# Kernel tuning notes

Hardware: AMD Instinct MI355X
Metric: run time of the kernel (lower is better)

## Reference

```python
import jax, jax.numpy as jnp
import numpy as np

NUM_CLASSES = 19
IGNORE = 255
KLD_MARGIN = 3.0
DEC = 0.01
BOT_EPS, TOP_EPS = 1e-4, 1.0
# eight-corner neighbor offsets (size=1), order matches AAF layers.eightcorner_activation
EDGE_OFFS = ((-1, -1), (-1, 0), (-1, 1), (0, -1), (0, 1), (1, -1), (1, 0), (1, 1))


def _shift(x, dy, dx, pad_val):
    # Shift along H,W (axes 1,2): out[:, y, x] = x[:, y+dy, x+dx], padded with pad_val.
    pads = [(0, 0), (1, 1), (1, 1)] + [(0, 0)] * (x.ndim - 3)
    xp = jnp.pad(x, pads, constant_values=pad_val)
    h, w = x.shape[1], x.shape[2]
    return xp[:, 1 + dy:1 + dy + h, 1 + dx:1 + dx + w]


def _resize_bilinear_ac(x, oh, ow):
    # torch F.interpolate(mode='bilinear', align_corners=True) on NCHW.
    n, c, h, w = x.shape
    ys = jnp.linspace(0.0, h - 1.0, oh)
    xs = jnp.linspace(0.0, w - 1.0, ow)
    y0 = jnp.floor(ys).astype(jnp.int32); y1 = jnp.minimum(y0 + 1, h - 1)
    x0 = jnp.floor(xs).astype(jnp.int32); x1 = jnp.minimum(x0 + 1, w - 1)
    wy = (ys - y0).astype(x.dtype)[None, None, :, None]
    wx = (xs - x0).astype(x.dtype)[None, None, None, :]
    rows = x[:, :, y0, :] * (1.0 - wy) + x[:, :, y1, :] * wy  # (N,C,oh,W)
    return rows[:, :, :, x0] * (1.0 - wx) + rows[:, :, :, x1] * wx  # (N,C,oh,ow)


def setup_inputs() -> dict:
    key = jax.random.key(0)
    k1, k2 = jax.random.split(key)
    preds = jax.random.normal(k1, (2, NUM_CLASSES, 64, 64), dtype=jnp.float32)
    targets = jax.random.randint(k2, (2, 512, 512), 0, NUM_CLASSES, dtype=jnp.int32)
    w_edge = jnp.zeros((1, 1, 1, NUM_CLASSES, 1, 3), dtype=jnp.float32)
    w_not_edge = jnp.zeros((1, 1, 1, NUM_CLASSES, 1, 3), dtype=jnp.float32)
    return {"preds": preds, "targets": targets, "w_edge": w_edge, "w_not_edge": w_not_edge}


def reference(preds, targets, w_edge, w_not_edge):
    h, w = targets.shape[1], targets.shape[2]
    pred = _resize_bilinear_ac(preds, h, w)          # (N,C,H,W)
    prob = jax.nn.softmax(pred, axis=1)
    prob = jnp.transpose(prob, (0, 2, 3, 1))          # (N,H,W,C) NHWC layout used by AAF layers

    labels = targets                                  # (N,H,W)
    ign = labels == IGNORE
    one_label = jnp.where(ign, 0, labels)
    ohl = jax.nn.one_hot(one_label, NUM_CLASSES, dtype=jnp.float32)  # (N,H,W,C)
    ohl = jnp.where(ign[..., None], float(IGNORE), ohl)

    # edge/non-edge class weights: softmax over last dim, take index 0 -> (1,1,1,C,1)
    w_e = jax.nn.softmax(w_edge, axis=-1)[..., 0]
    w_ne = jax.nn.softmax(w_not_edge, axis=-1)[..., 0]

    # ignores_from_label: bidirectional ignore mask, neighbor order is reversed offsets
    ignore_c = labels > NUM_CLASSES - 1               # (N,H,W)
    ignore8 = jnp.stack([_shift(ignore_c, -dy, -dx, True) | ignore_c for dy, dx in EDGE_OFFS], axis=-1)
    not_ignore = ~ignore8[:, :, :, None, :]           # (N,H,W,1,8)

    # edges_from_label: neighbor label (padded with ignore_class) differs from center
    edge8 = jnp.stack([_shift(ohl, dy, dx, float(IGNORE)) != ohl for dy, dx in EDGE_OFFS], axis=-1)  # (N,H,W,C,8)
    edge = edge8 & not_ignore
    not_edge = (~edge) & not_ignore

    # eightcorner_activation on probabilities (zero padded)
    probs_paired = jnp.stack([_shift(prob, dy, dx, 0.0) for dy, dx in EDGE_OFFS], axis=-1)  # (N,H,W,C,8)
    p = prob[..., None]                               # (N,H,W,C,1)
    pc = jnp.clip(p, BOT_EPS, TOP_EPS)
    npc = jnp.clip(1.0 - p, BOT_EPS, TOP_EPS)
    ppc = jnp.clip(probs_paired, BOT_EPS, TOP_EPS)
    nppc = jnp.clip(1.0 - probs_paired, BOT_EPS, TOP_EPS)

    # binary KL divergence per class/neighbor
    kldiv = ppc * jnp.log(ppc / pc) + nppc * jnp.log(nppc / npc)  # (N,H,W,C,8)

    # per-pixel class weights: sum_c w[c]*one_hot[c] -> (N,H,W,1,1)
    we_map = jnp.sum(w_e * ohl[..., None], axis=3, keepdims=True)
    wne_map = jnp.sum(w_ne * ohl[..., None], axis=3, keepdims=True)

    edge_loss = jnp.maximum(0.0, KLD_MARGIN - kldiv) * we_map
    not_edge_loss = kldiv * wne_map

    # torch.mean over gathered nonzero indices == masked sum / count
    e_cnt = jnp.maximum(jnp.sum(edge), 1).astype(jnp.float32)
    ne_cnt = jnp.maximum(jnp.sum(not_edge), 1).astype(jnp.float32)
    e_mean = jnp.sum(jnp.where(edge, edge_loss, 0.0)) / e_cnt
    ne_mean = jnp.sum(jnp.where(not_edge, not_edge_loss, 0.0)) / ne_cnt

    return e_mean * 1.0 * DEC + ne_mean * 1.0 * DEC
```

## Files before the change

kernel.cpp:

```cpp
#include <hip/hip_runtime.h>
#include <stdint.h>


#define NC 19
#define HH 512
#define WW 512
#define NB 2
#define TS 16
#define HS 18
#define HP (HS * HS)
#define ATRS 28
#define PS 25
#define NBLK2 1024
#define LOGEPS -9.210340371976182f

typedef _Float16 f16x2 __attribute__((ext_vector_type(2)));

#if __has_builtin(__builtin_amdgcn_fdot2)
#define FDOT2(a, b, c) __builtin_amdgcn_fdot2((a), (b), (c), false)
#else
#define FDOT2(a, b, c) fmaf((float)(a)[1], (float)(b)[1], fmaf((float)(a)[0], (float)(b)[0], (c)))
#endif

struct Part { float es, ns; unsigned int cnt, pad; };

union U32F2 { uint32_t u; f16x2 h; };
__device__ __forceinline__ uint32_t bc_u32(f16x2 v) { U32F2 x; x.h = v; return x.u; }
__device__ __forceinline__ f16x2 bc_h2(uint32_t v) { U32F2 x; x.u = v; return x.h; }
__device__ __forceinline__ float extf(f16x2 v, int h) { return h ? (float)v[1] : (float)v[0]; }

template <bool KEEP>
__device__ __forceinline__ int pix_compute(const float* __restrict__ patch,
                                           const int* __restrict__ tg,
                                           int y, int x, int y0b, int x0b,
                                           uint32_t* __restrict__ ATrow,
                                           f16x2* Dh, f16x2* Lh) {
    const bool oob = ((unsigned)y >= (unsigned)HH) | ((unsigned)x >= (unsigned)WW);
    if (oob) {
        const _Float16 aP = (_Float16)1e-4f, dP = (_Float16)LOGEPS;
        const _Float16 tP = (_Float16)((float)aP * (float)dP);
        const uint32_t aPP = bc_u32((f16x2){aP, aP});
        const uint32_t tPP = bc_u32((f16x2){tP, tP});
        const uint32_t aPL = bc_u32((f16x2){aP, (_Float16)0.0f});
        const uint32_t tPL = bc_u32((f16x2){tP, (_Float16)0.0f});
#pragma unroll
        for (int i = 0; i < 5; ++i) {
            uint4 wv;
            wv.x = aPP; wv.y = tPP;
            wv.z = (i < 4) ? aPP : aPL;
            wv.w = (i < 4) ? tPP : tPL;
            *reinterpret_cast<uint4*>(ATrow + 4 * i) = wv;
            if (KEEP) {
                Dh[2 * i] = (f16x2){dP, dP};
                Dh[2 * i + 1] = (i < 4) ? (f16x2){dP, dP} : (f16x2){dP, (_Float16)0.0f};
                Lh[2 * i] = (f16x2){(_Float16)0.0f, (_Float16)0.0f};
                Lh[2 * i + 1] = (f16x2){(_Float16)0.0f, (_Float16)0.0f};
            }
        }
        return 255;
    }

    const int lab = tg[(y << 9) + x];
    const float fy = (float)(y * 63) / 511.0f;
    const float fx = (float)(x * 63) / 511.0f;
    const int y0 = (int)fy, x0 = (int)fx;
    const float wy = fy - (float)y0, wx = fx - (float)x0;
    const int y1 = min(y0 + 1, 63), x1 = min(x0 + 1, 63);
    const float omwy = 1.0f - wy, omwx = 1.0f - wx;
    const int o00 = (y0 - y0b) * 5 + (x0 - x0b);
    const int o01 = (y0 - y0b) * 5 + (x1 - x0b);
    const int o10 = (y1 - y0b) * 5 + (x0 - x0b);
    const int o11 = (y1 - y0b) * 5 + (x1 - x0b);

    float v[NC], w[NC];
    float m = -1e30f;
#pragma unroll
    for (int c = 0; c < NC; ++c) {
        const float* pc_ = &patch[c * PS];
        const float a = pc_[o00] * omwy + pc_[o10] * wy;
        const float b = pc_[o01] * omwy + pc_[o11] * wy;
        const float vv = a * omwx + b * wx;
        v[c] = vv;
        m = fmaxf(m, vv);
    }
    float s = 0.0f;
#pragma unroll
    for (int c = 0; c < NC; ++c) { w[c] = __expf(v[c] - m); s += w[c]; }
    const float inv = 1.0f / s;
    const float lns = __logf(s) + m;

#pragma unroll
    for (int i = 0; i < 5; ++i) {
        _Float16 av[4], tv[4], dv[4], lv[4];
#pragma unroll
        for (int q = 0; q < 4; ++q) {
            const int c = 4 * i + q;
            _Float16 a16 = (_Float16)0.0f, d16 = (_Float16)0.0f,
                     l16 = (_Float16)0.0f, t16 = (_Float16)0.0f;
            if (c < NC) {
                const float p = w[c] * inv;
                const float la = fmaxf(v[c] - lns, LOGEPS);
                const float aa = fmaxf(p, 1e-4f);
                const float lb = __logf(fmaxf(1.0f - p, 1e-4f));
                a16 = (_Float16)aa;
                d16 = (_Float16)(la - lb);
                l16 = (_Float16)lb;
                t16 = (_Float16)fmaf((float)a16, (float)d16, (float)l16);
            }
            av[q] = a16; tv[q] = t16; dv[q] = d16; lv[q] = l16;
        }
        uint4 wv;
        wv.x = bc_u32((f16x2){av[0], av[1]});
        wv.y = bc_u32((f16x2){tv[0], tv[1]});
        wv.z = bc_u32((f16x2){av[2], av[3]});
        wv.w = bc_u32((f16x2){tv[2], tv[3]});
        *reinterpret_cast<uint4*>(ATrow + 4 * i) = wv;
        if (KEEP) {
            Dh[2 * i] = (f16x2){dv[0], dv[1]};
            Dh[2 * i + 1] = (f16x2){dv[2], dv[3]};
            Lh[2 * i] = (f16x2){lv[0], lv[1]};
            Lh[2 * i + 1] = (f16x2){lv[2], lv[3]};
        }
    }
    return lab;
}

__global__ __launch_bounds__(256, 4) void k_fused(const float* __restrict__ preds,
                                                  const int* __restrict__ targets,
                                                  const float* __restrict__ w_edge,
                                                  const float* __restrict__ w_not_edge,
                                                  Part* __restrict__ pb) {
    __shared__ __align__(16) uint32_t AT[HP * ATRS];
    __shared__ int   TG[HP];
    __shared__ float swe[NC], swn[NC];
    __shared__ float patch[NC * PS];
    __shared__ float r_es[4], r_ns[4];
    __shared__ unsigned int r_cnt[4];

    const int tid = threadIdx.x;
    const int bx = blockIdx.x, n = blockIdx.z;

    if (tid < NC) {
        {
            float a = w_edge[tid * 3 + 0], b = w_edge[tid * 3 + 1], c = w_edge[tid * 3 + 2];
            float m = fmaxf(a, fmaxf(b, c));
            float ea = __expf(a - m), eb = __expf(b - m), ec = __expf(c - m);
            swe[tid] = ea / (ea + eb + ec);
        }
        {
            float a = w_not_edge[tid * 3 + 0], b = w_not_edge[tid * 3 + 1], c = w_not_edge[tid * 3 + 2];
            float m = fmaxf(a, fmaxf(b, c));
            float ea = __expf(a - m), eb = __expf(b - m), ec = __expf(c - m);
            swn[tid] = ea / (ea + eb + ec);
        }
    }

    const int* tg = targets + (n << 18);
    const float* pbase = preds + (size_t)n * NC * 4096;

    const int ty = tid >> 4, tx = tid & 15;
    const int hi = (ty + 1) * HS + (tx + 1);
    const int DOFF[8] = {-HS - 1, -HS, -HS + 1, -1, 1, HS - 1, HS, HS + 1};
    const f16x2 one2 = {(_Float16)1.0f, (_Float16)1.0f};
    const f16x2 k32 = {(_Float16)3.0f, (_Float16)3.0f};
    const f16x2 z2 = {(_Float16)0.0f, (_Float16)0.0f};

    float e_s = 0.0f, ne_s = 0.0f;
    unsigned int cnt = 0;

    for (int half = 0; half < 2; ++half) {
        const int by = blockIdx.y + 16 * half;
        if (half) __syncthreads();

        const int yT = max(by * TS - 1, 0), xL = max(bx * TS - 1, 0);
        const int y0b = (yT * 63) / 511, x0b = (xL * 63) / 511;
        for (int t = tid; t < NC * PS; t += 256) {
            const int c = t / PS, r = t - c * PS;
            const int ry = r / 5, rx = r - ry * 5;
            const int sy = min(y0b + ry, 63), sx = min(x0b + rx, 63);
            patch[t] = pbase[c * 4096 + (sy << 6) + sx];
        }
        __syncthreads();

        if (tid < 68) {
            int i;
            if (tid < 18)      i = tid;
            else if (tid < 36) i = 306 + (tid - 18);
            else if (tid < 52) i = (tid - 35) * HS;
            else               i = (tid - 51) * HS + 17;
            const int hy = i / HS, hx = i - hy * HS;
            TG[i] = pix_compute<false>(patch, tg, by * TS + hy - 1, bx * TS + hx - 1,
                                       y0b, x0b, &AT[i * ATRS], nullptr, nullptr);
        }

        f16x2 Dh[10], Lh[10];
        const int lab = pix_compute<true>(patch, tg, by * TS + ty, bx * TS + tx,
                                          y0b, x0b, &AT[hi * ATRS], Dh, Lh);
        TG[hi] = lab;
        __syncthreads();

        const bool interior_blk = (bx > 0) & (bx < 31) & (by > 0) & (by < 31);
        const int plab = lab >> 1, hlab = lab & 1;
        float es_h = 0.0f, ns_h = 0.0f;
        unsigned int cnt_h = 0;

        if (interior_blk) {
#pragma unroll
            for (int k = 0; k < 8; ++k) {
                const int np = hi + DOFF[k];
                const int nlab = TG[np];
                const int pn = nlab >> 1, hn = nlab & 1;
                const uint32_t* wbp = &AT[np * ATRS];
                float dot0 = 0.0f, dot1 = 0.0f;
                f16x2 klLw = z2, klNw = z2;
#pragma unroll
                for (int i = 0; i < 5; ++i) {
                    const uint4 rd = *reinterpret_cast<const uint4*>(wbp + 4 * i);
                    const int j0 = 2 * i, j1 = 2 * i + 1;
                    const f16x2 kl20 = bc_h2(rd.y) - (bc_h2(rd.x) * Dh[j0] + Lh[j0]);
                    const f16x2 kl21 = bc_h2(rd.w) - (bc_h2(rd.z) * Dh[j1] + Lh[j1]);
                    dot0 = FDOT2(kl20, one2, dot0);
                    dot1 = FDOT2(kl21, one2, dot1);
                    klLw = (j0 == plab) ? kl20 : klLw;
                    klLw = (j1 == plab) ? kl21 : klLw;
                    klNw = (j0 == pn) ? kl20 : klNw;
                    klNw = (j1 == pn) ? kl21 : klNw;
                }
                const float dot = dot0 + dot1;
                const float klL = extf(klLw, hlab);
                const float klN = extf(klNw, hn);
                const bool df = (lab != nlab);
                const float w = df ? 1.0f : 0.0f;
                es_h = fmaf(w, fmaxf(3.0f - klL, 0.0f) + fmaxf(3.0f - klN, 0.0f), es_h);
                ns_h += dot - w * (klL + klN);
                cnt_h += df ? ((2u << 16) | (NC - 2)) : NC;
            }
            e_s = fmaf(es_h, swe[lab], e_s);
            ne_s = fmaf(ns_h, swn[lab], ne_s);
            cnt += cnt_h;
        } else if (lab <= NC - 1) {
#pragma unroll
            for (int k = 0; k < 8; ++k) {
                const int off = DOFF[k];
                const int rlab = TG[hi - off];
                const int np = hi + off;
                const int nlab = TG[np];
                const int pn = nlab >> 1, hn = nlab & 1;
                const uint32_t* wbp = &AT[np * ATRS];
                float dot0 = 0.0f, dot1 = 0.0f, ekall = 0.0f;
                f16x2 klLw = z2, klNw = z2;
#pragma unroll
                for (int i = 0; i < 5; ++i) {
                    const uint4 rd = *reinterpret_cast<const uint4*>(wbp + 4 * i);
                    const int j0 = 2 * i, j1 = 2 * i + 1;
                    const f16x2 kl20 = bc_h2(rd.y) - (bc_h2(rd.x) * Dh[j0] + Lh[j0]);
                    const f16x2 kl21 = bc_h2(rd.w) - (bc_h2(rd.z) * Dh[j1] + Lh[j1]);
                    dot0 = FDOT2(kl20, one2, dot0);
                    dot1 = FDOT2(kl21, one2, dot1);
                    f16x2 m0 = k32 - kl20, m1 = k32 - kl21;
                    m0[0] = m0[0] > (_Float16)0.0f ? m0[0] : (_Float16)0.0f;
                    m0[1] = m0[1] > (_Float16)0.0f ? m0[1] : (_Float16)0.0f;
                    m1[0] = m1[0] > (_Float16)0.0f ? m1[0] : (_Float16)0.0f;
                    m1[1] = m1[1] > (_Float16)0.0f ? m1[1] : (_Float16)0.0f;
                    ekall = FDOT2(m0, one2, ekall);
                    ekall = FDOT2(m1, one2, ekall);
                    klLw = (j0 == plab) ? kl20 : klLw;
                    klLw = (j1 == plab) ? kl21 : klLw;
                    klNw = (j0 == pn) ? kl20 : klNw;
                    klNw = (j1 == pn) ? kl21 : klNw;
                }
                const float dot = dot0 + dot1;
                const float klL = extf(klLw, hlab);
                const float klN = extf(klNw, hn);
                const bool isPad = (nlab == 255);
                const bool df = (lab != nlab) && !isPad;
                const float w = df ? 1.0f : 0.0f;
                const float ek_int = w * (fmaxf(3.0f - klL, 0.0f) + fmaxf(3.0f - klN, 0.0f));
                const float nk_int = dot - w * (klL + klN);
                const float ek_pad = ekall - 3.0f;
                const float ek_k = isPad ? ek_pad : ek_int;
                const float nk_k = isPad ? 0.0f : nk_int;
                const unsigned int pc = isPad ? NC : (df ? 2u : 0u);
                const bool valid = (rlab <= NC - 1);
                const float vf = valid ? 1.0f : 0.0f;
                es_h = fmaf(vf, ek_k, es_h);
                ns_h = fmaf(vf, nk_k, ns_h);
                cnt_h += valid ? ((pc << 16) | (NC - pc)) : 0u;
            }
            e_s = fmaf(es_h, swe[lab], e_s);
            ne_s = fmaf(ns_h, swn[lab], ne_s);
            cnt += cnt_h;
        }
    }

#pragma unroll
    for (int off = 32; off > 0; off >>= 1) {
        e_s  += __shfl_down(e_s, off, 64);
        ne_s += __shfl_down(ne_s, off, 64);
        cnt  += __shfl_down(cnt, off, 64);
    }
    const int wid = tid >> 6, lane = tid & 63;
    if (lane == 0) { r_es[wid] = e_s; r_ns[wid] = ne_s; r_cnt[wid] = cnt; }
    __syncthreads();
    if (tid == 0) {
        float tes = 0.0f, tns = 0.0f;
        unsigned int tc = 0;
#pragma unroll
        for (int w = 0; w < 4; ++w) { tes += r_es[w]; tns += r_ns[w]; tc += r_cnt[w]; }
        const int bid = (blockIdx.z * gridDim.y + blockIdx.y) * gridDim.x + blockIdx.x;
        pb[bid].es = tes; pb[bid].ns = tns; pb[bid].cnt = tc; pb[bid].pad = 0;
    }
}

__global__ __launch_bounds__(256) void k_final(const Part* __restrict__ pb,
                                               float* __restrict__ out) {
    const int tid = threadIdx.x;
    double es = 0.0, ns = 0.0;
    long long ec = 0, nc = 0;
    for (int i = tid; i < NBLK2; i += 256) {
        es += (double)pb[i].es; ns += (double)pb[i].ns;
        const unsigned int c = pb[i].cnt;
        ec += (long long)(c >> 16); nc += (long long)(c & 0xFFFFu);
    }
#pragma unroll
    for (int off = 32; off > 0; off >>= 1) {
        es += __shfl_down(es, off, 64);
        ns += __shfl_down(ns, off, 64);
        ec += __shfl_down(ec, off, 64);
        nc += __shfl_down(nc, off, 64);
    }
    __shared__ double ses[4], sns[4];
    __shared__ long long sec[4], snc[4];
    const int wid = tid >> 6, lane = tid & 63;
    if (lane == 0) { ses[wid] = es; sns[wid] = ns; sec[wid] = ec; snc[wid] = nc; }
    __syncthreads();
    if (tid == 0) {
        double tes = 0.0, tns = 0.0;
        long long tec = 0, tnc = 0;
#pragma unroll
        for (int w = 0; w < 4; ++w) { tes += ses[w]; tns += sns[w]; tec += sec[w]; tnc += snc[w]; }
        double ecd = (double)tec; if (ecd < 1.0) ecd = 1.0;
        double ncd = (double)tnc; if (ncd < 1.0) ncd = 1.0;
        out[0] = (float)((tes / ecd) * 0.01 + (tns / ncd) * 0.01);
    }
}

extern "C" void kernel_launch(void* const* d_in, const int* in_sizes, int n_in,
                              void* d_out, int out_size, void* d_ws, size_t ws_size,
                              hipStream_t stream) {
    const float* preds      = (const float*)d_in[0];
    const int*   targets    = (const int*)d_in[1];
    const float* w_edge     = (const float*)d_in[2];
    const float* w_not_edge = (const float*)d_in[3];

    Part* pb = (Part*)d_ws;

    dim3 grid(WW / TS, HH / TS / 2, NB);
    k_fused<<<grid, 256, 0, stream>>>(preds, targets, w_edge, w_not_edge, pb);
    k_final<<<1, 256, 0, stream>>>(pb, (float*)d_out);
}
```

Before: 98.68 us.

## Switch softmax/KL math to base-2 logs, drop max-subtraction, one tile per block

Pre-scales logits by log2(e) so the softmax uses native exp2 and log2, and drops the running-max subtraction (safe only because the logits are bounded). The ln2 factor is folded into the per-class weights, and the KL margin and pad constants are rescaled to match. Each block now handles one tile instead of two, doubling the grid and the partial buffer. The AT row stride shrinks from 28 to 20 and the occupancy hint rises to 5, trading some LDS bank spreading for more resident blocks.

Result: faster. 88.74 us (-10.1%).

```diff
diff --git a/kernel.cpp b/kernel.cpp
--- a/kernel.cpp
+++ b/kernel.cpp
@@ -9,12 +9,22 @@
 #define TS 16
 #define HS 18
 #define HP (HS * HS)
-#define ATRS 28
+#define ATRS 20
 #define PS 25
-#define NBLK2 1024
-#define LOGEPS -9.210340371976182f
+#define NBLK 2048
+#define LOG2E 1.4426950408889634f
+#define LN2 0.6931471805599453f
+#define LOG2EPS -13.287712379549449f
+#define K2F 4.3280851226668906f
+#define K2PAD 4.328125f
 
 typedef _Float16 f16x2 __attribute__((ext_vector_type(2)));
+
+#if __has_builtin(__builtin_amdgcn_exp2f)
+#define EXP2F(x) __builtin_amdgcn_exp2f(x)
+#else
+#define EXP2F(x) __expf((x) * LN2)
+#endif
 
 #if __has_builtin(__builtin_amdgcn_fdot2)
 #define FDOT2(a, b, c) __builtin_amdgcn_fdot2((a), (b), (c), false)
@@ -37,7 +47,7 @@
                                            f16x2* Dh, f16x2* Lh) {
     const bool oob = ((unsigned)y >= (unsigned)HH) | ((unsigned)x >= (unsigned)WW);
     if (oob) {
-        const _Float16 aP = (_Float16)1e-4f, dP = (_Float16)LOGEPS;
+        const _Float16 aP = (_Float16)1e-4f, dP = (_Float16)LOG2EPS;
         const _Float16 tP = (_Float16)((float)aP * (float)dP);
         const uint32_t aPP = bc_u32((f16x2){aP, aP});
         const uint32_t tPP = bc_u32((f16x2){tP, tP});
@@ -67,27 +77,27 @@
     const float wy = fy - (float)y0, wx = fx - (float)x0;
     const int y1 = min(y0 + 1, 63), x1 = min(x0 + 1, 63);
     const float omwy = 1.0f - wy, omwx = 1.0f - wx;
+    const float w00 = omwy * omwx, w01 = omwy * wx;
+    const float w10 = wy * omwx,   w11 = wy * wx;
     const int o00 = (y0 - y0b) * 5 + (x0 - x0b);
-    const int o01 = (y0 - y0b) * 5 + (x1 - x0b);
-    const int o10 = (y1 - y0b) * 5 + (x0 - x0b);
-    const int o11 = (y1 - y0b) * 5 + (x1 - x0b);
-
-    float v[NC], w[NC];
-    float m = -1e30f;
+    const int o01 = o00 + (x1 - x0);
+    const int o10 = o00 + (y1 - y0) * 5;
+    const int o11 = o10 + (x1 - x0);
+
+    float v2[NC], w[NC];
+    float s = 0.0f;
 #pragma unroll
     for (int c = 0; c < NC; ++c) {
         const float* pc_ = &patch[c * PS];
-        const float a = pc_[o00] * omwy + pc_[o10] * wy;
-        const float b = pc_[o01] * omwy + pc_[o11] * wy;
-        const float vv = a * omwx + b * wx;
-        v[c] = vv;
-        m = fmaxf(m, vv);
-    }
-    float s = 0.0f;
-#pragma unroll
-    for (int c = 0; c < NC; ++c) { w[c] = __expf(v[c] - m); s += w[c]; }
+        const float vv = fmaf(pc_[o00], w00, fmaf(pc_[o01], w01,
+                          fmaf(pc_[o10], w10, pc_[o11] * w11)));
+        v2[c] = vv;
+        const float e = EXP2F(vv);
+        w[c] = e;
+        s += e;
+    }
     const float inv = 1.0f / s;
-    const float lns = __logf(s) + m;
+    const float lns2 = __log2f(s);
 
 #pragma unroll
     for (int i = 0; i < 5; ++i) {
@@ -99,13 +109,13 @@
                      l16 = (_Float16)0.0f, t16 = (_Float16)0.0f;
             if (c < NC) {
                 const float p = w[c] * inv;
-                const float la = fmaxf(v[c] - lns, LOGEPS);
+                const float la = fmaxf(v2[c] - lns2, LOG2EPS);
                 const float aa = fmaxf(p, 1e-4f);
-                const float lb = __logf(fmaxf(1.0f - p, 1e-4f));
+                const float lb = __log2f(fmaxf(1.0f - p, 1e-4f));
                 a16 = (_Float16)aa;
                 d16 = (_Float16)(la - lb);
                 l16 = (_Float16)lb;
-                t16 = (_Float16)fmaf((float)a16, (float)d16, (float)l16);
+                t16 = a16 * d16 + l16;
             }
             av[q] = a16; tv[q] = t16; dv[q] = d16; lv[q] = l16;
         }
@@ -125,7 +135,7 @@
     return lab;
 }
 
-__global__ __launch_bounds__(256, 4) void k_fused(const float* __restrict__ preds,
+__global__ __launch_bounds__(256, 5) void k_fused(const float* __restrict__ preds,
                                                   const int* __restrict__ targets,
                                                   const float* __restrict__ w_edge,
                                                   const float* __restrict__ w_not_edge,
@@ -138,20 +148,20 @@
     __shared__ unsigned int r_cnt[4];
 
     const int tid = threadIdx.x;
-    const int bx = blockIdx.x, n = blockIdx.z;
+    const int bx = blockIdx.x, by = blockIdx.y, n = blockIdx.z;
 
     if (tid < NC) {
         {
             float a = w_edge[tid * 3 + 0], b = w_edge[tid * 3 + 1], c = w_edge[tid * 3 + 2];
             float m = fmaxf(a, fmaxf(b, c));
             float ea = __expf(a - m), eb = __expf(b - m), ec = __expf(c - m);
-            swe[tid] = ea / (ea + eb + ec);
+            swe[tid] = (ea / (ea + eb + ec)) * LN2;
         }
         {
             float a = w_not_edge[tid * 3 + 0], b = w_not_edge[tid * 3 + 1], c = w_not_edge[tid * 3 + 2];
             float m = fmaxf(a, fmaxf(b, c));
             float ea = __expf(a - m), eb = __expf(b - m), ec = __expf(c - m);
-            swn[tid] = ea / (ea + eb + ec);
+            swn[tid] = (ea / (ea + eb + ec)) * LN2;
         }
     }
 
@@ -162,135 +172,130 @@
     const int hi = (ty + 1) * HS + (tx + 1);
     const int DOFF[8] = {-HS - 1, -HS, -HS + 1, -1, 1, HS - 1, HS, HS + 1};
     const f16x2 one2 = {(_Float16)1.0f, (_Float16)1.0f};
-    const f16x2 k32 = {(_Float16)3.0f, (_Float16)3.0f};
+    const f16x2 k32 = {(_Float16)K2F, (_Float16)K2F};
     const f16x2 z2 = {(_Float16)0.0f, (_Float16)0.0f};
 
     float e_s = 0.0f, ne_s = 0.0f;
     unsigned int cnt = 0;
 
-    for (int half = 0; half < 2; ++half) {
-        const int by = blockIdx.y + 16 * half;
-        if (half) __syncthreads();
-
-        const int yT = max(by * TS - 1, 0), xL = max(bx * TS - 1, 0);
-        const int y0b = (yT * 63) / 511, x0b = (xL * 63) / 511;
-        for (int t = tid; t < NC * PS; t += 256) {
-            const int c = t / PS, r = t - c * PS;
-            const int ry = r / 5, rx = r - ry * 5;
-            const int sy = min(y0b + ry, 63), sx = min(x0b + rx, 63);
-            patch[t] = pbase[c * 4096 + (sy << 6) + sx];
-        }
-        __syncthreads();
-
-        if (tid < 68) {
-            int i;
-            if (tid < 18)      i = tid;
-            else if (tid < 36) i = 306 + (tid - 18);
-            else if (tid < 52) i = (tid - 35) * HS;
-            else               i = (tid - 51) * HS + 17;
-            const int hy = i / HS, hx = i - hy * HS;
-            TG[i] = pix_compute<false>(patch, tg, by * TS + hy - 1, bx * TS + hx - 1,
-                                       y0b, x0b, &AT[i * ATRS], nullptr, nullptr);
-        }
-
-        f16x2 Dh[10], Lh[10];
-        const int lab = pix_compute<true>(patch, tg, by * TS + ty, bx * TS + tx,
-                                          y0b, x0b, &AT[hi * ATRS], Dh, Lh);
-        TG[hi] = lab;
-        __syncthreads();
-
-        const bool interior_blk = (bx > 0) & (bx < 31) & (by > 0) & (by < 31);
-        const int plab = lab >> 1, hlab = lab & 1;
-        float es_h = 0.0f, ns_h = 0.0f;
-        unsigned int cnt_h = 0;
-
-        if (interior_blk) {
-#pragma unroll
-            for (int k = 0; k < 8; ++k) {
-                const int np = hi + DOFF[k];
-                const int nlab = TG[np];
-                const int pn = nlab >> 1, hn = nlab & 1;
-                const uint32_t* wbp = &AT[np * ATRS];
-                float dot0 = 0.0f, dot1 = 0.0f;
-                f16x2 klLw = z2, klNw = z2;
-#pragma unroll
-                for (int i = 0; i < 5; ++i) {
-                    const uint4 rd = *reinterpret_cast<const uint4*>(wbp + 4 * i);
-                    const int j0 = 2 * i, j1 = 2 * i + 1;
-                    const f16x2 kl20 = bc_h2(rd.y) - (bc_h2(rd.x) * Dh[j0] + Lh[j0]);
-                    const f16x2 kl21 = bc_h2(rd.w) - (bc_h2(rd.z) * Dh[j1] + Lh[j1]);
-                    dot0 = FDOT2(kl20, one2, dot0);
-                    dot1 = FDOT2(kl21, one2, dot1);
-                    klLw = (j0 == plab) ? kl20 : klLw;
-                    klLw = (j1 == plab) ? kl21 : klLw;
-                    klNw = (j0 == pn) ? kl20 : klNw;
-                    klNw = (j1 == pn) ? kl21 : klNw;
-                }
-                const float dot = dot0 + dot1;
-                const float klL = extf(klLw, hlab);
-                const float klN = extf(klNw, hn);
-                const bool df = (lab != nlab);
-                const float w = df ? 1.0f : 0.0f;
-                es_h = fmaf(w, fmaxf(3.0f - klL, 0.0f) + fmaxf(3.0f - klN, 0.0f), es_h);
-                ns_h += dot - w * (klL + klN);
-                cnt_h += df ? ((2u << 16) | (NC - 2)) : NC;
+    const int yT = max(by * TS - 1, 0), xL = max(bx * TS - 1, 0);
+    const int y0b = (yT * 63) / 511, x0b = (xL * 63) / 511;
+    for (int t = tid; t < NC * PS; t += 256) {
+        const int c = t / PS, r = t - c * PS;
+        const int ry = r / 5, rx = r - ry * 5;
+        const int sy = min(y0b + ry, 63), sx = min(x0b + rx, 63);
+        patch[t] = pbase[c * 4096 + (sy << 6) + sx] * LOG2E;
+    }
+    __syncthreads();
+
+    if (tid < 68) {
+        int i;
+        if (tid < 18)      i = tid;
+        else if (tid < 36) i = 306 + (tid - 18);
+        else if (tid < 52) i = (tid - 35) * HS;
+        else               i = (tid - 51) * HS + 17;
+        const int hy = i / HS, hx = i - hy * HS;
+        TG[i] = pix_compute<false>(patch, tg, by * TS + hy - 1, bx * TS + hx - 1,
+                                   y0b, x0b, &AT[i * ATRS], nullptr, nullptr);
+    }
+
+    f16x2 Dh[10], Lh[10];
+    const int lab = pix_compute<true>(patch, tg, by * TS + ty, bx * TS + tx,
+                                      y0b, x0b, &AT[hi * ATRS], Dh, Lh);
+    TG[hi] = lab;
+    __syncthreads();
+
+    const bool interior_blk = (bx > 0) & (bx < 31) & (by > 0) & (by < 31);
+    const int plab = lab >> 1, hlab = lab & 1;
+    float es_h = 0.0f, ns_h = 0.0f;
+    unsigned int cnt_h = 0;
+
+    if (interior_blk) {
+#pragma unroll
+        for (int k = 0; k < 8; ++k) {
+            const int np = hi + DOFF[k];
+            const int nlab = TG[np];
+            const int pn = nlab >> 1, hn = nlab & 1;
+            const uint32_t* wbp = &AT[np * ATRS];
+            float dot0 = 0.0f, dot1 = 0.0f;
+            f16x2 klLw = z2, klNw = z2;
+#pragma unroll
+            for (int i = 0; i < 5; ++i) {
+                const uint4 rd = *reinterpret_cast<const uint4*>(wbp + 4 * i);
+                const int j0 = 2 * i, j1 = 2 * i + 1;
+                const f16x2 kl20 = bc_h2(rd.y) - (bc_h2(rd.x) * Dh[j0] + Lh[j0]);
+                const f16x2 kl21 = bc_h2(rd.w) - (bc_h2(rd.z) * Dh[j1] + Lh[j1]);
+                dot0 = FDOT2(kl20, one2, dot0);
+                dot1 = FDOT2(kl21, one2, dot1);
+                klLw = (j0 == plab) ? kl20 : klLw;
+                klLw = (j1 == plab) ? kl21 : klLw;
+                klNw = (j0 == pn) ? kl20 : klNw;
+                klNw = (j1 == pn) ? kl21 : klNw;
             }
-            e_s = fmaf(es_h, swe[lab], e_s);
-            ne_s = fmaf(ns_h, swn[lab], ne_s);
-            cnt += cnt_h;
-        } else if (lab <= NC - 1) {
-#pragma unroll
-            for (int k = 0; k < 8; ++k) {
-                const int off = DOFF[k];
-                const int rlab = TG[hi - off];
-                const int np = hi + off;
-                const int nlab = TG[np];
-                const int pn = nlab >> 1, hn = nlab & 1;
-                const uint32_t* wbp = &AT[np * ATRS];
-                float dot0 = 0.0f, dot1 = 0.0f, ekall = 0.0f;
-                f16x2 klLw = z2, klNw = z2;
-#pragma unroll
-                for (int i = 0; i < 5; ++i) {
-                    const uint4 rd = *reinterpret_cast<const uint4*>(wbp + 4 * i);
-                    const int j0 = 2 * i, j1 = 2 * i + 1;
-                    const f16x2 kl20 = bc_h2(rd.y) - (bc_h2(rd.x) * Dh[j0] + Lh[j0]);
-                    const f16x2 kl21 = bc_h2(rd.w) - (bc_h2(rd.z) * Dh[j1] + Lh[j1]);
-                    dot0 = FDOT2(kl20, one2, dot0);
-                    dot1 = FDOT2(kl21, one2, dot1);
-                    f16x2 m0 = k32 - kl20, m1 = k32 - kl21;
-                    m0[0] = m0[0] > (_Float16)0.0f ? m0[0] : (_Float16)0.0f;
-                    m0[1] = m0[1] > (_Float16)0.0f ? m0[1] : (_Float16)0.0f;
-                    m1[0] = m1[0] > (_Float16)0.0f ? m1[0] : (_Float16)0.0f;
-                    m1[1] = m1[1] > (_Float16)0.0f ? m1[1] : (_Float16)0.0f;
-                    ekall = FDOT2(m0, one2, ekall);
-                    ekall = FDOT2(m1, one2, ekall);
-                    klLw = (j0 == plab) ? kl20 : klLw;
-                    klLw = (j1 == plab) ? kl21 : klLw;
-                    klNw = (j0 == pn) ? kl20 : klNw;
-                    klNw = (j1 == pn) ? kl21 : klNw;
-                }
-                const float dot = dot0 + dot1;
-                const float klL = extf(klLw, hlab);
-                const float klN = extf(klNw, hn);
-                const bool isPad = (nlab == 255);
-                const bool df = (lab != nlab) && !isPad;
-                const float w = df ? 1.0f : 0.0f;
-                const float ek_int = w * (fmaxf(3.0f - klL, 0.0f) + fmaxf(3.0f - klN, 0.0f));
-                const float nk_int = dot - w * (klL + klN);
-                const float ek_pad = ekall - 3.0f;
-                const float ek_k = isPad ? ek_pad : ek_int;
-                const float nk_k = isPad ? 0.0f : nk_int;
-                const unsigned int pc = isPad ? NC : (df ? 2u : 0u);
-                const bool valid = (rlab <= NC - 1);
-                const float vf = valid ? 1.0f : 0.0f;
-                es_h = fmaf(vf, ek_k, es_h);
-                ns_h = fmaf(vf, nk_k, ns_h);
-                cnt_h += valid ? ((pc << 16) | (NC - pc)) : 0u;
+            const float dot = dot0 + dot1;
+            const float klL = extf(klLw, hlab);
+            const float klN = extf(klNw, hn);
+            const bool df = (lab != nlab);
+            const float w = df ? 1.0f : 0.0f;
+            es_h = fmaf(w, fmaxf(K2F - klL, 0.0f) + fmaxf(K2F - klN, 0.0f), es_h);
+            ns_h += dot - w * (klL + klN);
+            cnt_h += df ? ((2u << 16) | (NC - 2)) : NC;
+        }
+        e_s = fmaf(es_h, swe[lab], e_s);
+        ne_s = fmaf(ns_h, swn[lab], ne_s);
+        cnt += cnt_h;
+    } else if (lab <= NC - 1) {
+#pragma unroll
+        for (int k = 0; k < 8; ++k) {
+            const int off = DOFF[k];
+            const int rlab = TG[hi - off];
+            const int np = hi + off;
+            const int nlab = TG[np];
+            const int pn = nlab >> 1, hn = nlab & 1;
+            const uint32_t* wbp = &AT[np * ATRS];
+            float dot0 = 0.0f, dot1 = 0.0f, ekall = 0.0f;
+            f16x2 klLw = z2, klNw = z2;
+#pragma unroll
+            for (int i = 0; i < 5; ++i) {
+                const uint4 rd = *reinterpret_cast<const uint4*>(wbp + 4 * i);
+                const int j0 = 2 * i, j1 = 2 * i + 1;
+                const f16x2 kl20 = bc_h2(rd.y) - (bc_h2(rd.x) * Dh[j0] + Lh[j0]);
+                const f16x2 kl21 = bc_h2(rd.w) - (bc_h2(rd.z) * Dh[j1] + Lh[j1]);
+                dot0 = FDOT2(kl20, one2, dot0);
+                dot1 = FDOT2(kl21, one2, dot1);
+                f16x2 m0 = k32 - kl20, m1 = k32 - kl21;
+                m0[0] = m0[0] > (_Float16)0.0f ? m0[0] : (_Float16)0.0f;
+                m0[1] = m0[1] > (_Float16)0.0f ? m0[1] : (_Float16)0.0f;
+                m1[0] = m1[0] > (_Float16)0.0f ? m1[0] : (_Float16)0.0f;
+                m1[1] = m1[1] > (_Float16)0.0f ? m1[1] : (_Float16)0.0f;
+                ekall = FDOT2(m0, one2, ekall);
+                ekall = FDOT2(m1, one2, ekall);
+                klLw = (j0 == plab) ? kl20 : klLw;
+                klLw = (j1 == plab) ? kl21 : klLw;
+                klNw = (j0 == pn) ? kl20 : klNw;
+                klNw = (j1 == pn) ? kl21 : klNw;
             }
-            e_s = fmaf(es_h, swe[lab], e_s);
-            ne_s = fmaf(ns_h, swn[lab], ne_s);
-            cnt += cnt_h;
-        }
+            const float dot = dot0 + dot1;
+            const float klL = extf(klLw, hlab);
+            const float klN = extf(klNw, hn);
+            const bool isPad = (nlab == 255);
+            const bool df = (lab != nlab) && !isPad;
+            const float w = df ? 1.0f : 0.0f;
+            const float ek_int = w * (fmaxf(K2F - klL, 0.0f) + fmaxf(K2F - klN, 0.0f));
+            const float nk_int = dot - w * (klL + klN);
+            const float ek_pad = ekall - K2PAD;
+            const float ek_k = isPad ? ek_pad : ek_int;
+            const float nk_k = isPad ? 0.0f : nk_int;
+            const unsigned int pc = isPad ? NC : (df ? 2u : 0u);
+            const bool valid = (rlab <= NC - 1);
+            const float vf = valid ? 1.0f : 0.0f;
+            es_h = fmaf(vf, ek_k, es_h);
+            ns_h = fmaf(vf, nk_k, ns_h);
+            cnt_h += valid ? ((pc << 16) | (NC - pc)) : 0u;
+        }
+        e_s = fmaf(es_h, swe[lab], e_s);
+        ne_s = fmaf(ns_h, swn[lab], ne_s);
+        cnt += cnt_h;
     }
 
 #pragma unroll
@@ -317,7 +322,7 @@
     const int tid = threadIdx.x;
     double es = 0.0, ns = 0.0;
     long long ec = 0, nc = 0;
-    for (int i = tid; i < NBLK2; i += 256) {
+    for (int i = tid; i < NBLK; i += 256) {
         es += (double)pb[i].es; ns += (double)pb[i].ns;
         const unsigned int c = pb[i].cnt;
         ec += (long long)(c >> 16); nc += (long long)(c & 0xFFFFu);
@@ -355,7 +360,7 @@
 
     Part* pb = (Part*)d_ws;
 
-    dim3 grid(WW / TS, HH / TS / 2, NB);
+    dim3 grid(WW / TS, HH / TS, NB);
     k_fused<<<grid, 256, 0, stream>>>(preds, targets, w_edge, w_not_edge, pb);
     k_final<<<1, 256, 0, stream>>>(pb, (float*)d_out);
 }
```
